# Optimization experiments

Hardware: AMD Instinct MI355X
Metric: run time of the kernel (lower is better)

The kernel has to match this reference:

```python
import jax, jax.numpy as jnp
import numpy as np

DIM = 1024
SEQ_LEN = 4096
K = 256
HEADS = 16
DIM_HEAD = DIM // HEADS  # 64
BATCH = 4


def setup_inputs() -> dict:
    key = jax.random.key(0)
    ks = jax.random.split(key, 8)
    x = jax.random.normal(ks[0], (BATCH, SEQ_LEN, DIM), dtype=jnp.float32)
    # nn.Linear weights are [out, in]; y = x @ W.T
    std_lin = 1.0 / np.sqrt(DIM)
    Wq = jax.random.uniform(ks[1], (HEADS * DIM_HEAD, DIM), minval=-std_lin, maxval=std_lin, dtype=jnp.float32)
    Wk = jax.random.uniform(ks[2], (HEADS * DIM_HEAD, DIM), minval=-std_lin, maxval=std_lin, dtype=jnp.float32)
    Wv = jax.random.uniform(ks[3], (HEADS * DIM_HEAD, DIM), minval=-std_lin, maxval=std_lin, dtype=jnp.float32)
    # proj_k/proj_v init_: uniform(-1/sqrt(k), 1/sqrt(k)) on [seq_len, k]
    std_p = 1.0 / np.sqrt(K)
    proj_k = jax.random.uniform(ks[4], (SEQ_LEN, K), minval=-std_p, maxval=std_p, dtype=jnp.float32)
    proj_v = jax.random.uniform(ks[5], (SEQ_LEN, K), minval=-std_p, maxval=std_p, dtype=jnp.float32)
    std_o = 1.0 / np.sqrt(HEADS * DIM_HEAD)
    Wo = jax.random.uniform(ks[6], (DIM, HEADS * DIM_HEAD), minval=-std_o, maxval=std_o, dtype=jnp.float32)
    bo = jax.random.uniform(ks[7], (DIM,), minval=-std_o, maxval=std_o, dtype=jnp.float32)
    return {"x": x, "Wq": Wq, "Wk": Wk, "Wv": Wv, "proj_k": proj_k, "proj_v": proj_v, "Wo": Wo, "bo": bo}


def reference(x, Wq, Wk, Wv, proj_k, proj_v, Wo, bo):
    b, n, d = x.shape
    h, dh, k = HEADS, DIM_HEAD, K
    # q/k/v projections
    q = jnp.einsum('bnd,ed->bne', x, Wq)            # [b, n, h*dh]
    keys = jnp.einsum('bnd,ed->bne', x, Wk)         # [b, n, h*dh]
    vals = jnp.einsum('bnd,ed->bne', x, Wv)         # [b, n, h*dh]
    # low-rank projection along sequence: [b, n, e] x [n, k] -> [b, k, e]
    keys = jnp.einsum('bne,nk->bke', keys, proj_k[:n])
    vals = jnp.einsum('bne,nk->bke', vals, proj_v[:n])
    # split heads
    q = q.reshape(b, n, h, dh).transpose(0, 2, 1, 3)        # [b, h, n, dh]
    keys = keys.reshape(b, k, h, dh).transpose(0, 2, 1, 3)  # [b, h, k, dh]
    vals = vals.reshape(b, k, h, dh).transpose(0, 2, 1, 3)  # [b, h, k, dh]
    dots = jnp.einsum('bhnd,bhkd->bhnk', q, keys) * (dh ** -0.5)
    attn = jax.nn.softmax(dots, axis=-1)
    out = jnp.einsum('bhnk,bhkd->bhnd', attn, vals)
    out = out.transpose(0, 2, 1, 3).reshape(b, n, h * dh)
    return jnp.einsum('bne,oe->bno', out, Wo) + bo
```

## Files before the change

### kernel.cpp

```cpp
#include <hip/hip_runtime.h>
#include <hip/hip_bf16.h>
#include <stdint.h>

typedef unsigned short u16;
typedef __attribute__((ext_vector_type(8))) short bf16x8;
typedef __attribute__((ext_vector_type(4))) float f32x4;

#define DEV __device__ __forceinline__

DEV u16 f2bf(float f) {
  union { float f; unsigned u; } v; v.f = f;
  unsigned r = (v.u + 0x7fffu + ((v.u >> 16) & 1u)) >> 16;
  return (u16)r;
}

DEV unsigned pk2(float lo, float hi) {
  union { __hip_bfloat162 h; unsigned u; } c;
  c.h = __float22bfloat162_rn(make_float2(lo, hi));
  return c.u;
}

DEV f32x4 mfma16(bf16x8 a, bf16x8 b, f32x4 c) {
  return __builtin_amdgcn_mfma_f32_16x16x32_bf16(a, b, c, 0, 0, 0);
}

DEV void gload_lds16(const u16* g, u16* l) {
  __builtin_amdgcn_global_load_lds((const __attribute__((address_space(1))) void*)g,
                                   (__attribute__((address_space(3))) void*)l, 16, 0, 0);
}

#define QSCALE 0.18033688011112042f

__global__ void cvt_xpose_kernel(const float* __restrict__ src, u16* __restrict__ dst_rm,
                                 u16* __restrict__ dst_tp, int R, int C,
                                 long zS, long zRM, long zTP) {
  __shared__ u16 tile[64][72];
  src += (size_t)blockIdx.z * zS;
  dst_tp += (size_t)blockIdx.z * zTP;
  int r0 = blockIdx.y * 64, c0 = blockIdx.x * 64;
  int tr = threadIdx.x >> 2, tc = (threadIdx.x & 3) * 16;
  const float* s = src + (size_t)(r0 + tr) * C + c0 + tc;
  u16 loc[16];
#pragma unroll
  for (int q = 0; q < 4; ++q) {
    float4 v = ((const float4*)s)[q];
    loc[q * 4 + 0] = f2bf(v.x); loc[q * 4 + 1] = f2bf(v.y);
    loc[q * 4 + 2] = f2bf(v.z); loc[q * 4 + 3] = f2bf(v.w);
  }
#pragma unroll
  for (int i = 0; i < 16; ++i) tile[tr][tc + i] = loc[i];
  if (dst_rm) {
    u16* d = dst_rm + (size_t)blockIdx.z * zRM + (size_t)(r0 + tr) * C + c0 + tc;
    *(bf16x8*)d = *(const bf16x8*)&loc[0];
    *(bf16x8*)(d + 8) = *(const bf16x8*)&loc[8];
  }
  __syncthreads();
  u16 tmp[16];
#pragma unroll
  for (int i = 0; i < 16; ++i) tmp[i] = tile[tc + i][tr];
  u16* d = dst_tp + (size_t)(c0 + tr) * R + r0 + tc;
  *(bf16x8*)d = *(const bf16x8*)&tmp[0];
  *(bf16x8*)(d + 8) = *(const bf16x8*)&tmp[8];
}

__global__ void cvt_w4_kernel(const float* __restrict__ s0, const float* __restrict__ s1,
                              const float* __restrict__ s2, const float* __restrict__ s3,
                              u16* __restrict__ d0, u16* __restrict__ d1,
                              u16* __restrict__ d2, u16* __restrict__ d3) {
  const float* s; u16* d;
  switch (blockIdx.y) {
    case 0: s = s0; d = d0; break;
    case 1: s = s1; d = d1; break;
    case 2: s = s2; d = d2; break;
    default: s = s3; d = d3; break;
  }
  int i = blockIdx.x * 256 + threadIdx.x;
  float4 v = ((const float4*)s)[i];
  ushort4 o; o.x = f2bf(v.x); o.y = f2bf(v.y); o.z = f2bf(v.z); o.w = f2bf(v.w);
  ((ushort4*)d)[i] = o;
}

__global__ void reduce4_kernel(const float* __restrict__ part, u16* __restrict__ out) {
  int i = blockIdx.x * 256 + threadIdx.x;
  const float4* p = (const float4*)part;
  float4 a = p[i], b = p[i + 524288], c = p[i + 1048576], d = p[i + 1572864];
  ushort4 o;
  o.x = f2bf(a.x + b.x + c.x + d.x);
  o.y = f2bf(a.y + b.y + c.y + d.y);
  o.z = f2bf(a.z + b.z + c.z + d.z);
  o.w = f2bf(a.w + b.w + c.w + d.w);
  ((ushort4*)out)[i] = o;
}

template<int OMODE>
__global__ __launch_bounds__(256, 4)
void gemm_bt_kernel(const u16* __restrict__ A, const u16* __restrict__ Bt,
                    const u16* __restrict__ Bt2, void* __restrict__ Cout,
                    u16* __restrict__ CoutT, const float* __restrict__ bias, float cscale,
                    int ldA, int ldB, int ldC, int Klen,
                    long zA, long zB, long zC, int bMod, long kChunk) {
  __shared__ __align__(16) u16 smA[2][128 * 32];
  __shared__ __align__(16) u16 smB[2][128 * 32];
  const int t = threadIdx.x;
  const int lane = t & 63, wave = t >> 6;
  const int wm = wave & 1, wn = wave >> 1;
  const int g = lane >> 4, r = lane & 15;
  const int id = (blockIdx.y << 3) | blockIdx.x;
  const int s = (id & 7) * gridDim.y + (id >> 3);
  const int bx = s & 7, by = s >> 3;
  const int z = blockIdx.z;
  const int b = z % bMod, kc = z / bMod;
  const u16* Ab = A + (size_t)b * zA + (size_t)kc * kChunk;
  const u16* Bbase = (Bt2 && (b & 1)) ? Bt2 : Bt;
  const u16* Bb = Bbase + (size_t)b * zB + (size_t)kc * kChunk;
  const int m0 = by * 128, n0 = bx * 128;
  const int srow = t >> 2;
  const int lslot = ((t & 3) + 4 - ((srow >> 1) & 3)) & 3;

  f32x4 acc[4][4];
#pragma unroll
  for (int m = 0; m < 4; ++m)
#pragma unroll
    for (int n = 0; n < 4; ++n) acc[m][n] = f32x4{0.f, 0.f, 0.f, 0.f};

  auto STAGE = [&](int buf, int k0) {
#pragma unroll
    for (int p = 0; p < 2; ++p) {
      int row = p * 64 + srow;
      gload_lds16(Ab + (size_t)(m0 + row) * ldA + k0 + lslot * 8, &smA[buf][p * 2048 + wave * 512]);
      gload_lds16(Bb + (size_t)(n0 + row) * ldB + k0 + lslot * 8, &smB[buf][p * 2048 + wave * 512]);
    }
  };

  const int nt = Klen >> 5;
  STAGE(0, 0);
  __syncthreads();
  int cur = 0;
  for (int it = 0; it < nt; ++it) {
    if (it + 1 < nt) STAGE(cur ^ 1, (it + 1) << 5);
    bf16x8 af[4], bfr[4];
#pragma unroll
    for (int m = 0; m < 4; ++m) {
      int row = wm * 64 + m * 16 + r;
      int ps = (g + (row >> 1)) & 3;
      af[m] = *(const bf16x8*)&smA[cur][row * 32 + ps * 8];
    }
#pragma unroll
    for (int n = 0; n < 4; ++n) {
      int row = wn * 64 + n * 16 + r;
      int ps = (g + (row >> 1)) & 3;
      bfr[n] = *(const bf16x8*)&smB[cur][row * 32 + ps * 8];
    }
#pragma unroll
    for (int m = 0; m < 4; ++m)
#pragma unroll
      for (int n = 0; n < 4; ++n)
        acc[m][n] = mfma16(af[m], bfr[n], acc[m][n]);
    __syncthreads();
    cur ^= 1;
  }

  if constexpr (OMODE == 0) {
    u16* C = (u16*)Cout + (size_t)z * zC;
#pragma unroll
    for (int n = 0; n < 4; ++n) {
      int col = n0 + wn * 64 + n * 16 + r;
#pragma unroll
      for (int m = 0; m < 4; ++m) {
        int rowb = m0 + wm * 64 + m * 16 + 4 * g;
#pragma unroll
        for (int rr = 0; rr < 4; ++rr)
          C[(size_t)(rowb + rr) * ldC + col] = f2bf(acc[m][n][rr] * cscale);
      }
    }
  } else if constexpr (OMODE == 3) {
    if ((z & 1) == 0) {
      u16* C = (u16*)Cout + (size_t)(z >> 1) * zC;
#pragma unroll
      for (int n = 0; n < 4; ++n) {
        int col = n0 + wn * 64 + n * 16 + r;
#pragma unroll
        for (int m = 0; m < 4; ++m) {
          int rowb = m0 + wm * 64 + m * 16 + 4 * g;
#pragma unroll
          for (int rr = 0; rr < 4; ++rr)
            C[(size_t)(rowb + rr) * ldC + col] = f2bf(acc[m][n][rr]);
        }
      }
    } else {
      u16* C = CoutT + (size_t)(z >> 1) * zC;
#pragma unroll
      for (int n = 0; n < 4; ++n) {
        int col = n0 + wn * 64 + n * 16 + r;
#pragma unroll
        for (int m = 0; m < 4; ++m) {
          int rowb = m0 + wm * 64 + m * 16 + 4 * g;
          ushort4 o;
          o.x = f2bf(acc[m][n][0]); o.y = f2bf(acc[m][n][1]);
          o.z = f2bf(acc[m][n][2]); o.w = f2bf(acc[m][n][3]);
          *(ushort4*)&C[(size_t)col * 256 + rowb] = o;
        }
      }
    }
  } else {
    float* C = (float*)Cout + (size_t)z * zC;
#pragma unroll
    for (int n = 0; n < 4; ++n) {
      int col = n0 + wn * 64 + n * 16 + r;
      float bv = (OMODE == 1) ? bias[col] : 0.f;
#pragma unroll
      for (int m = 0; m < 4; ++m) {
        int rowb = m0 + wm * 64 + m * 16 + 4 * g;
#pragma unroll
        for (int rr = 0; rr < 4; ++rr)
          C[(size_t)(rowb + rr) * ldC + col] = acc[m][n][rr] + bv;
      }
    }
  }
}

__global__ __launch_bounds__(256, 4)
void attn_kernel(const u16* __restrict__ Q, const u16* __restrict__ Kl,
                 const u16* __restrict__ VT, u16* __restrict__ Out) {
  __shared__ __align__(16) u16 sm[20480];
  const int t = threadIdx.x, lane = t & 63, w = t >> 6;
  const int g = lane >> 4, r = lane & 15;
  const int id = (blockIdx.y << 6) | blockIdx.x;
  const int s = (id & 7) * (gridDim.y << 3) + (id >> 3);
  const int b = blockIdx.z, h = s >> 6, n0 = (s & 63) * 64;
  const u16* Kb = Kl + (size_t)b * 262144 + h * 64;
  const u16* Vb = VT + (size_t)b * 262144 + (size_t)(h * 64) * 256;
  u16* vbase = sm + 16384;

  const int vd = t >> 2;
  const int vsl = (t & 3) ^ (vd & 3);
  auto stage_slice = [&](int kk, int buf) {
    gload_lds16(Vb + (size_t)vd * 256 + kk * 32 + vsl * 8, vbase + buf * 2048 + w * 512);
  };

#pragma unroll
  for (int p = 0; p < 8; ++p) {
    int row = p * 32 + (t >> 3);
    int ls = ((t & 7) + 8 - (row & 7)) & 7;
    gload_lds16(Kb + (size_t)row * 1024 + ls * 8, sm + p * 2048 + w * 512);
  }
  stage_slice(0, 0);
  stage_slice(1, 1);
  const int qrow = n0 + w * 16 + r;
  const u16* Qp = Q + ((size_t)(b * 4096 + qrow)) * 1024 + h * 64 + g * 8;
  bf16x8 aq0 = *(const bf16x8*)Qp;
  bf16x8 aq1 = *(const bf16x8*)(Qp + 32);
  __syncthreads();

  f32x4 dotv[16];
#pragma unroll
  for (int kf = 0; kf < 16; ++kf) {
    int row = kf * 16 + r;
    bf16x8 kb0 = *(const bf16x8*)&sm[row * 64 + ((g + row) & 7) * 8];
    bf16x8 kb1 = *(const bf16x8*)&sm[row * 64 + ((4 + g + row) & 7) * 8];
    f32x4 d = f32x4{0.f, 0.f, 0.f, 0.f};
    d = mfma16(kb0, aq0, d);
    d = mfma16(kb1, aq1, d);
    dotv[kf] = d;
  }
  __syncthreads();

  float mx = -3.4e38f;
#pragma unroll
  for (int kf = 0; kf < 16; ++kf)
    mx = fmaxf(mx, fmaxf(fmaxf(dotv[kf][0], dotv[kf][1]), fmaxf(dotv[kf][2], dotv[kf][3])));
  mx = fmaxf(mx, __shfl_xor(mx, 16, 64));
  mx = fmaxf(mx, __shfl_xor(mx, 32, 64));
  float ssum = 0.f;
#pragma unroll
  for (int kf = 0; kf < 16; ++kf)
#pragma unroll
    for (int j = 0; j < 4; ++j) {
      float p = exp2f(dotv[kf][j] - mx);
      dotv[kf][j] = p;
      ssum += p;
    }
  ssum += __shfl_xor(ssum, 16, 64);
  ssum += __shfl_xor(ssum, 32, 64);
  const float inv = 1.f / ssum;

  const int q16 = w * 16 + r;
  const int qx = (q16 & 7) << 3;
#pragma unroll
  for (int kf = 0; kf < 16; ++kf) {
    uint2 val;
    val.x = pk2(dotv[kf][0] * inv, dotv[kf][1] * inv);
    val.y = pk2(dotv[kf][2] * inv, dotv[kf][3] * inv);
    *(uint2*)&sm[(q16 * 256 + kf * 16 + 4 * g) ^ qx] = val;
  }

  f32x4 oacc[4];
#pragma unroll
  for (int df = 0; df < 4; ++df) oacc[df] = f32x4{0.f, 0.f, 0.f, 0.f};
#pragma unroll
  for (int kk = 0; kk < 8; ++kk) {
    bf16x8 ap = *(const bf16x8*)&sm[(q16 * 256 + kk * 32 + g * 8) ^ qx];
    const u16* vb = vbase + (kk & 1) * 2048;
#pragma unroll
    for (int df = 0; df < 4; ++df) {
      int d = df * 16 + r;
      bf16x8 bv = *(const bf16x8*)&vb[d * 32 + (g ^ (d & 3)) * 8];
      oacc[df] = mfma16(ap, bv, oacc[df]);
    }
    if (kk < 7) {
      __syncthreads();
      if (kk < 6) stage_slice(kk + 2, kk & 1);
    }
  }
#pragma unroll
  for (int df = 0; df < 4; ++df)
#pragma unroll
    for (int rr = 0; rr < 4; ++rr) {
      int orow = n0 + w * 16 + 4 * g + rr;
      int ocol = h * 64 + df * 16 + r;
      Out[((size_t)(b * 4096 + orow)) * 1024 + ocol] = f2bf(oacc[df][rr]);
    }
}

extern "C" void kernel_launch(void* const* d_in, const int* in_sizes, int n_in,
                              void* d_out, int out_size, void* d_ws, size_t ws_size,
                              hipStream_t stream) {
  const float* x  = (const float*)d_in[0];
  const float* Wq = (const float*)d_in[1];
  const float* Wk = (const float*)d_in[2];
  const float* Wv = (const float*)d_in[3];
  const float* pk = (const float*)d_in[4];
  const float* pv = (const float*)d_in[5];
  const float* Wo = (const float*)d_in[6];
  const float* bo = (const float*)d_in[7];

  u16* ws = (u16*)d_ws;
  u16* xbf   = ws;
  u16* xT    = xbf + 16777216;
  u16* wqb   = xT + 16777216;
  u16* wkb   = wqb + 1048576;
  u16* wvb   = wkb + 1048576;
  u16* wob   = wvb + 1048576;
  u16* projT = wob + 1048576;
  u16* Qb    = projT + 2097152;
  u16* xp    = Qb + 16777216;
  u16* klow  = xp + 2097152;
  u16* vT    = klow + 1048576;
  u16* aout  = xbf;
  float* xp_part = (float*)Qb;

  cvt_xpose_kernel<<<dim3(16, 64, 4), 256, 0, stream>>>(x, xbf, xT, 4096, 1024,
                                                        4194304, 4194304, 4194304);
  cvt_w4_kernel<<<dim3(1024, 4), 256, 0, stream>>>(Wq, Wk, Wv, Wo, wqb, wkb, wvb, wob);
  cvt_xpose_kernel<<<dim3(4, 64, 1), 256, 0, stream>>>(pk, nullptr, projT, 4096, 256, 0, 0, 0);
  cvt_xpose_kernel<<<dim3(4, 64, 1), 256, 0, stream>>>(pv, nullptr, projT + 1048576, 4096, 256, 0, 0, 0);
  gemm_bt_kernel<2><<<dim3(8, 4, 16), 256, 0, stream>>>(
      projT, xT, nullptr, (void*)xp_part, nullptr, nullptr, 1.f,
      4096, 4096, 1024, 1024, 0, 4194304, 524288, 4, 1024);
  reduce4_kernel<<<2048, 256, 0, stream>>>(xp_part, xp);
  gemm_bt_kernel<3><<<dim3(8, 2, 8), 256, 0, stream>>>(
      xp, wkb, wvb, (void*)klow, vT, nullptr, 1.f,
      1024, 1024, 1024, 1024, 262144, 0, 262144, 8, 0);
  gemm_bt_kernel<0><<<dim3(8, 128, 1), 256, 0, stream>>>(
      xbf, wqb, nullptr, (void*)Qb, nullptr, nullptr, QSCALE,
      1024, 1024, 1024, 1024, 0, 0, 0, 1, 0);
  attn_kernel<<<dim3(64, 16, 4), 256, 0, stream>>>(Qb, klow, vT, aout);
  gemm_bt_kernel<1><<<dim3(8, 128, 1), 256, 0, stream>>>(
      aout, wob, nullptr, d_out, nullptr, bo, 1.f,
      1024, 1024, 1024, 1024, 0, 0, 0, 1, 0);
}
```

Before: 221.7 us.

## Use 256x256-tile 8-wave GEMM with phased double-buffered pipeline for Q and output projections

Adds a new GEMM kernel with 256x256 output tiles, 512 threads, and a 128KB LDS double buffer. Each 64-wide K step is split into four phases, and the next tiles' global-to-LDS loads are interleaved with the MFMA work, using priority bumps and explicit vmcnt waits. It replaces the 128x128 GEMM for the Q projection and the Wo output projection, aiming for more data reuse per tile and better overlap of loads with compute. The trade-off is one block per CU and only 256 blocks over the 16384x1024 output, so fewer waves are in flight to hide latency and tail effects may grow.

```diff
diff --git a/kernel.cpp b/kernel.cpp
--- a/kernel.cpp
+++ b/kernel.cpp
@@ -219,6 +219,138 @@
   }
 }
 
+#define PHASE(bA, bB, MH, NH, STAGE_STMT, WAITMODE)                                     \
+  do {                                                                                  \
+    bf16x8 af[4][2], bfv[2][2];                                                         \
+    _Pragma("unroll")                                                                   \
+    for (int mi = 0; mi < 4; ++mi) {                                                    \
+      const u16* rp = (bA) + ((MH) * 128 + aoff + mi * 16) * 64;                        \
+      af[mi][0] = *(const bf16x8*)&rp[(g ^ rm) * 8];                                    \
+      af[mi][1] = *(const bf16x8*)&rp[((4 + g) ^ rm) * 8];                              \
+    }                                                                                   \
+    _Pragma("unroll")                                                                   \
+    for (int ni = 0; ni < 2; ++ni) {                                                    \
+      const u16* rp = (bB) + ((NH) * 128 + boff + ni * 16) * 64;                        \
+      bfv[ni][0] = *(const bf16x8*)&rp[(g ^ rm) * 8];                                   \
+      bfv[ni][1] = *(const bf16x8*)&rp[((4 + g) ^ rm) * 8];                             \
+    }                                                                                   \
+    STAGE_STMT;                                                                         \
+    __builtin_amdgcn_s_barrier();                                                       \
+    __builtin_amdgcn_sched_barrier(0);                                                  \
+    __builtin_amdgcn_s_setprio(1);                                                      \
+    _Pragma("unroll")                                                                   \
+    for (int mi = 0; mi < 4; ++mi)                                                      \
+      _Pragma("unroll")                                                                 \
+      for (int ni = 0; ni < 2; ++ni) {                                                  \
+        acc[(MH)*4+mi][(NH)*2+ni] = mfma16(af[mi][0], bfv[ni][0], acc[(MH)*4+mi][(NH)*2+ni]); \
+        acc[(MH)*4+mi][(NH)*2+ni] = mfma16(af[mi][1], bfv[ni][1], acc[(MH)*4+mi][(NH)*2+ni]); \
+      }                                                                                 \
+    __builtin_amdgcn_s_setprio(0);                                                      \
+    if ((WAITMODE) == 1) asm volatile("s_waitcnt vmcnt(4)" ::: "memory");               \
+    if ((WAITMODE) == 2) asm volatile("s_waitcnt vmcnt(0)" ::: "memory");               \
+    __builtin_amdgcn_s_barrier();                                                       \
+    __builtin_amdgcn_sched_barrier(0);                                                  \
+  } while (0)
+
+template<int OMODE>
+__global__ __launch_bounds__(512, 1)
+void gemm256_kernel(const u16* __restrict__ A, const u16* __restrict__ Bt,
+                    void* __restrict__ Cout, const float* __restrict__ bias,
+                    float cscale, int ldA, int ldB, int ldC, int Klen) {
+  __shared__ __align__(16) u16 lds[65536];
+  const int t = threadIdx.x;
+  const int lane = t & 63, wave = t >> 6;
+  const int g = lane >> 4, r = lane & 15, rm = r & 7;
+  const int wm = wave >> 2, wn = wave & 3;
+  const int id = blockIdx.y * 4 + blockIdx.x;
+  const int sw = (id & 7) * 32 + (id >> 3);
+  const int bx = sw & 3, by = sw >> 2;
+  const int m0 = by * 256, n0 = bx * 256;
+
+  const int trow = t >> 3, tslot = t & 7;
+  const int sslot = tslot ^ (trow & 7);
+  const u16* Asrc = A + (size_t)(m0 + trow) * ldA + sslot * 8;
+  const u16* Bsrc = Bt + sslot * 8;
+  const int bRow0 = n0 + (trow >> 5) * 64 + (trow & 31);
+  const int bRow1 = n0 + (2 + (trow >> 5)) * 64 + (trow & 31);
+
+  u16* const A0 = lds;
+  u16* const A1 = lds + 16384;
+  u16* const B0 = lds + 32768;
+  u16* const B1 = lds + 49152;
+
+  auto stageA = [&](u16* buf, int h, int k0) {
+    u16* d = buf + h * 8192 + t * 8;
+    const u16* s0 = Asrc + (size_t)(h * 64) * ldA + k0;
+    gload_lds16(s0, d);
+    gload_lds16(s0 + (size_t)128 * ldA, d + 4096);
+  };
+  auto stageB = [&](u16* buf, int h, int k0) {
+    u16* d = buf + h * 8192 + t * 8;
+    gload_lds16(Bsrc + (size_t)(bRow0 + h * 32) * ldB + k0, d);
+    gload_lds16(Bsrc + (size_t)(bRow1 + h * 32) * ldB + k0, d + 4096);
+  };
+
+  const int aoff = wm * 64 + r;
+  const int boff = wn * 32 + r;
+
+  f32x4 acc[8][4];
+#pragma unroll
+  for (int m = 0; m < 8; ++m)
+#pragma unroll
+    for (int n = 0; n < 4; ++n) acc[m][n] = f32x4{0.f, 0.f, 0.f, 0.f};
+
+  stageA(A0, 0, 0); stageB(B0, 0, 0); stageA(A0, 1, 0); stageB(B0, 1, 0);
+  stageA(A1, 0, 64); stageB(B1, 0, 64);
+  asm volatile("s_waitcnt vmcnt(4)" ::: "memory");
+  __builtin_amdgcn_s_barrier();
+  __builtin_amdgcn_sched_barrier(0);
+
+  const int nt = Klen >> 6;
+  for (int j = 0; j < (nt >> 1); ++j) {
+    const int ta = 2 * j, tb = ta + 1;
+    const int more = (ta + 2 < nt);
+    const int kb = tb * 64, kn = (ta + 2) * 64, kn2 = (tb + 2) * 64;
+    PHASE(A0, B0, 0, 0, stageA(A1, 1, kb), 0);
+    PHASE(A0, B0, 0, 1, stageB(B1, 1, kb), 0);
+    PHASE(A0, B0, 1, 0, if (more) stageA(A0, 0, kn), 0);
+    PHASE(A0, B0, 1, 1, if (more) stageB(B0, 0, kn), more ? 1 : 2);
+    PHASE(A1, B1, 0, 0, if (more) stageA(A0, 1, kn), 0);
+    PHASE(A1, B1, 0, 1, if (more) stageB(B0, 1, kn), 0);
+    PHASE(A1, B1, 1, 0, if (more) stageA(A1, 0, kn2), 0);
+    PHASE(A1, B1, 1, 1, if (more) stageB(B1, 0, kn2), more ? 1 : 2);
+  }
+
+  if constexpr (OMODE == 0) {
+    u16* C = (u16*)Cout;
+#pragma unroll
+    for (int n = 0; n < 4; ++n) {
+      int col = n0 + wn * 64 + n * 16 + r;
+#pragma unroll
+      for (int m = 0; m < 8; ++m) {
+        int rowb = m0 + wm * 128 + m * 16 + 4 * g;
+#pragma unroll
+        for (int rr = 0; rr < 4; ++rr)
+          C[(size_t)(rowb + rr) * ldC + col] = f2bf(acc[m][n][rr] * cscale);
+      }
+    }
+  } else {
+    float* C = (float*)Cout;
+#pragma unroll
+    for (int n = 0; n < 4; ++n) {
+      int col = n0 + wn * 64 + n * 16 + r;
+      float bv = bias[col];
+#pragma unroll
+      for (int m = 0; m < 8; ++m) {
+        int rowb = m0 + wm * 128 + m * 16 + 4 * g;
+#pragma unroll
+        for (int rr = 0; rr < 4; ++rr)
+          C[(size_t)(rowb + rr) * ldC + col] = acc[m][n][rr] + bv;
+      }
+    }
+  }
+}
+
 __global__ __launch_bounds__(256, 4)
 void attn_kernel(const u16* __restrict__ Q, const u16* __restrict__ Kl,
                  const u16* __restrict__ VT, u16* __restrict__ Out) {
@@ -361,11 +493,9 @@
   gemm_bt_kernel<3><<<dim3(8, 2, 8), 256, 0, stream>>>(
       xp, wkb, wvb, (void*)klow, vT, nullptr, 1.f,
       1024, 1024, 1024, 1024, 262144, 0, 262144, 8, 0);
-  gemm_bt_kernel<0><<<dim3(8, 128, 1), 256, 0, stream>>>(
-      xbf, wqb, nullptr, (void*)Qb, nullptr, nullptr, QSCALE,
-      1024, 1024, 1024, 1024, 0, 0, 0, 1, 0);
+  gemm256_kernel<0><<<dim3(4, 64), 512, 0, stream>>>(
+      xbf, wqb, (void*)Qb, nullptr, QSCALE, 1024, 1024, 1024, 1024);
   attn_kernel<<<dim3(64, 16, 4), 256, 0, stream>>>(Qb, klow, vT, aout);
-  gemm_bt_kernel<1><<<dim3(8, 128, 1), 256, 0, stream>>>(
-      aout, wob, nullptr, d_out, nullptr, bo, 1.f,
-      1024, 1024, 1024, 1024, 0, 0, 0, 1, 0);
-}
+  gemm256_kernel<1><<<dim3(4, 64), 512, 0, stream>>>(
+      aout, wob, d_out, bo, 1.f, 1024, 1024, 1024, 1024);
+}
```

New measurement: 226.1 us. Within noise of the previous version (+1.9%).
